# Performance work log

Measured on AMD Instinct MI355X. Metric: run time of the kernel, lower is better.

Reference implementation:

```python
import jax, jax.numpy as jnp
import numpy as np

STRIDE = 1
PADDING = 1

def setup_inputs() -> dict:
    key = jax.random.key(0)
    k1, k2 = jax.random.split(key)
    x = jax.random.normal(k1, (32, 128, 56, 56), dtype=jnp.float32)
    weight = jax.random.normal(k2, (256, 128, 3, 3), dtype=jnp.float32) * 0.01
    bias = jnp.zeros((256,), dtype=jnp.float32)
    return {"x": x, "weight": weight, "bias": bias}

def reference(x, weight, bias):
    # Same math as unfold (im2col) + matmul conv: a standard 2D cross-correlation.
    # Expressed as lax.conv_general_dilated, the efficient implicit-GEMM form.
    out = jax.lax.conv_general_dilated(
        x, weight,
        window_strides=(STRIDE, STRIDE),
        padding=[(PADDING, PADDING), (PADDING, PADDING)],
        dimension_numbers=("NCHW", "OIHW", "NCHW"),
    )
    out = out + bias[None, :, None, None]
    return out
```

## Files before the change

kernel.cpp:

```cpp
#include <hip/hip_runtime.h>

typedef int   v4i __attribute__((ext_vector_type(4)));
typedef float v4f __attribute__((ext_vector_type(4)));
typedef unsigned short ushort_t;

#define NB 32
#define CI 128
#define HW 56
#define KOC 256
#define HP 58
#define MTOT (NB*HW*HW)
#define XP_ELEMS ((size_t)NB*HP*HP*CI)
#define XP_OFF_BYTES ((size_t)1<<20)

__device__ __forceinline__ unsigned short f2bf(float f) {
    unsigned int u = __builtin_bit_cast(unsigned int, f);
    u += 0x7fffu + ((u >> 16) & 1u);
    return (unsigned short)(u >> 16);
}

__device__ __forceinline__ void gload16(const void* g, void* l) {
    __builtin_amdgcn_global_load_lds(
        (const __attribute__((address_space(1))) void*)g,
        (__attribute__((address_space(3))) void*)l, 16, 0, 0);
}

__global__ void wt_bf16(const float* __restrict__ w, ushort_t* __restrict__ wb) {
    int t = blockIdx.x * 256 + threadIdx.x;
    if (t >= KOC * CI) return;
    const float* src = w + (size_t)t * 9;
    int ko = t >> 7, c = t & 127;
    #pragma unroll
    for (int rs = 0; rs < 9; ++rs)
        wb[(size_t)(rs * KOC + ko) * CI + c] = f2bf(src[rs]);
}

__global__ void pad_nhwc_bf16(const float* __restrict__ x, ushort_t* __restrict__ xp) {
    __shared__ ushort_t tile[HW][136];
    int b = blockIdx.x;
    int n = b / HW, h = b % HW;
    int tid = threadIdx.x;
    const float* xr = x + (size_t)n * CI * HW * HW + (size_t)h * HW;
    for (int idx = tid; idx < CI * HW; idx += 256) {
        int c = idx / HW, w = idx % HW;
        tile[w][c] = f2bf(xr[(size_t)c * (HW * HW) + w]);
    }
    __syncthreads();
    ushort_t* xpr = xp + ((size_t)(n * HP + (h + 1)) * HP + 1) * CI;
    for (int idx = tid; idx < (HW * CI) / 8; idx += 256) {
        int w = idx >> 4, c8 = (idx & 15) * 8;
        *reinterpret_cast<uint4*>(xpr + (size_t)w * CI + c8) =
            *reinterpret_cast<const uint4*>(&tile[w][c8]);
    }
}

__global__ void border_zero(ushort_t* __restrict__ xp) {
    int t = blockIdx.x * 256 + threadIdx.x;
    if (t >= NB * 228 * 16) return;
    int c16 = t & 15;
    int p = (t >> 4) % 228;
    int n = t / (228 * 16);
    int h, wc;
    if (p < 58)       { h = 0;               wc = p; }
    else if (p < 116) { h = 57;              wc = p - 58; }
    else { int q = p - 116; h = 1 + (q >> 1); wc = (q & 1) * 57; }
    size_t off = ((size_t)(n * HP + h) * HP + wc) * CI + (size_t)c16 * 8;
    uint4 z; z.x = z.y = z.z = z.w = 0u;
    *reinterpret_cast<uint4*>(xp + off) = z;
}


#define BODY(POFF, IT, DO_STAGE) do {                                             \
    if (DO_STAGE) {                                                               \
        const int itn = (IT) + 1;                                                 \
        const int rsn = itn >> 2, cn = (itn & 3) * 32;                            \
        const int rn = (rsn * 11) >> 5, sn = rsn - rn * 3;                        \
        const size_t woffn = (size_t)rsn * (KOC * CI) + cn;                       \
        const size_t xoffn = (size_t)(rn * HP + sn) * CI + cn;                    \
        char* dst = ldsBase + ((POFF) ^ 16384);                                   \
        gload16(wb + wS0 + woffn, dst);                                           \
        gload16(wb + wS1 + woffn, dst + 4096);                                    \
        gload16(xp + xS0 + xoffn, dst + 8192);                                    \
        gload16(xp + xS1 + xoffn, dst + 12288);                                   \
    }                                                                             \
    _Pragma("unroll")                                                             \
    for (int a = 0; a < 4; ++a)                                                   \
        asm volatile("ds_read_b128 %0, %1 offset:" #POFF                          \
                     : "=v"(af[a]) : "v"(aAddr[a]));                              \
    _Pragma("unroll")                                                             \
    for (int b = 0; b < 4; ++b)                                                   \
        asm volatile("ds_read_b128 %0, %1 offset:" #POFF                          \
                     : "=v"(bf[b]) : "v"(bAddr[b]));                              \
    asm volatile("s_waitcnt lgkmcnt(0)");                                         \
    __builtin_amdgcn_sched_barrier(0);                                            \
    __builtin_amdgcn_s_setprio(1);                                                \
    _Pragma("unroll")                                                             \
    for (int a = 0; a < 4; ++a)                                                   \
        _Pragma("unroll")                                                         \
        for (int b = 0; b < 4; ++b)                                               \
            asm volatile("v_mfma_f32_16x16x32_bf16 %0, %1, %2, %0"                \
                         : "+v"(acc[a][b]) : "v"(af[a]), "v"(bf[b]));             \
    __builtin_amdgcn_s_setprio(0);                                                \
    asm volatile("s_waitcnt vmcnt(0)");                                           \
    __builtin_amdgcn_s_barrier();                                                 \
} while (0)

__global__ __launch_bounds__(256, 4) void conv_mfma(
    const ushort_t* __restrict__ xp,
    const ushort_t* __restrict__ wb,
    const float* __restrict__ bias,
    float* __restrict__ out)
{
    __shared__ alignas(16) ushort_t sAB[2][8192];

    const int tid  = threadIdx.x;
    const int lane = tid & 63;
    const int wv   = tid >> 6;
    const int wko  = wv >> 1, wm = wv & 1;
    const int bid   = blockIdx.x;
    const int chunk = (bid & 7) * 196 + (bid >> 3);
    const int mt = chunk >> 1, kt = chunk & 1;
    const int m0 = mt * 128, ko0 = kt * 128;
    const int lm = lane & 15, lk = lane >> 4;

    const int sc   = (lane & 3) ^ ((lane >> 3) & 3);
    const int row0 = wv * 16 + (lane >> 2);
    const size_t wS0 = (size_t)(ko0 + row0) * CI + sc * 8;
    const size_t wS1 = (size_t)(ko0 + 64 + row0) * CI + sc * 8;
    size_t xS0, xS1;
    {
        int mm = m0 + row0;
        int n = mm / 3136, tt = mm % 3136, oh = tt / 56, ow = tt % 56;
        xS0 = ((size_t)(n * HP + oh) * HP + ow) * CI + sc * 8;
        mm = m0 + 64 + row0;
        n = mm / 3136; tt = mm % 3136; oh = tt / 56; ow = tt % 56;
        xS1 = ((size_t)(n * HP + oh) * HP + ow) * CI + sc * 8;
    }
    char* ldsBase = (char*)&sAB[0][0] + wv * 1024;

    unsigned aAddr[4], bAddr[4];
    #pragma unroll
    for (int a = 0; a < 4; ++a) {
        int row = wko * 64 + a * 16 + lm;
        aAddr[a] = (unsigned)(size_t)&sAB[0][0]
                 + (unsigned)(row * 64 + (lk ^ ((row >> 1) & 3)) * 16);
    }
    #pragma unroll
    for (int b = 0; b < 4; ++b) {
        int row = wm * 64 + b * 16 + lm;
        bAddr[b] = (unsigned)(size_t)&sAB[0][0] + 8192u
                 + (unsigned)(row * 64 + (lk ^ ((row >> 1) & 3)) * 16);
    }

    v4f acc[4][4];
    const v4f vzero = {0.f, 0.f, 0.f, 0.f};
    #pragma unroll
    for (int a = 0; a < 4; ++a)
        #pragma unroll
        for (int b = 0; b < 4; ++b) acc[a][b] = vzero;

    v4i af[4], bf[4];

    gload16(wb + wS0, ldsBase);
    gload16(wb + wS1, ldsBase + 4096);
    gload16(xp + xS0, ldsBase + 8192);
    gload16(xp + xS1, ldsBase + 12288);
    asm volatile("s_waitcnt vmcnt(0)");
    __builtin_amdgcn_s_barrier();

    for (int t = 0; t < 17; ++t) {
        BODY(0,     2 * t,     true);
        BODY(16384, 2 * t + 1, true);
    }
    BODY(0,     34, true);
    BODY(16384, 35, false);

    asm volatile("s_nop 7\n\ts_nop 7\n\ts_nop 7"
        : "+v"(acc[0][0]), "+v"(acc[0][1]), "+v"(acc[0][2]), "+v"(acc[0][3]),
          "+v"(acc[1][0]), "+v"(acc[1][1]), "+v"(acc[1][2]), "+v"(acc[1][3]),
          "+v"(acc[2][0]), "+v"(acc[2][1]), "+v"(acc[2][2]), "+v"(acc[2][3]),
          "+v"(acc[3][0]), "+v"(acc[3][1]), "+v"(acc[3][2]), "+v"(acc[3][3]));

    const int koB = ko0 + wko * 64 + lk * 4;
    v4f bv[4];
    #pragma unroll
    for (int a = 0; a < 4; ++a)
        bv[a] = *reinterpret_cast<const v4f*>(bias + koB + a * 16);

    #pragma unroll
    for (int bb = 0; bb < 4; ++bb) {
        int mcol = m0 + wm * 64 + bb * 16 + lm;
        int n = mcol / 3136, t4 = mcol % 3136, oh = t4 / 56, ow = t4 % 56;
        size_t obase = (size_t)n * (KOC * 3136) + (size_t)oh * 56 + ow;
        #pragma unroll
        for (int a = 0; a < 4; ++a) {
            int kk = koB + a * 16;
            #pragma unroll
            for (int r = 0; r < 4; ++r)
                out[obase + (size_t)(kk + r) * 3136] = acc[a][bb][r] + bv[a][r];
        }
    }
}

__global__ void conv_naive(const float* __restrict__ x, const float* __restrict__ w,
                           const float* __restrict__ bias, float* __restrict__ out) {
    int idx = blockIdx.x * 256 + threadIdx.x;
    if (idx >= NB * KOC * HW * HW) return;
    int ow = idx % 56, t = idx / 56, oh = t % 56, t2 = t / 56, ko = t2 % 256, n = t2 / 256;
    float accv = bias[ko];
    for (int c = 0; c < CI; ++c)
        for (int r = 0; r < 3; ++r) {
            int ih = oh - 1 + r;
            if (ih < 0 || ih >= HW) continue;
            for (int s = 0; s < 3; ++s) {
                int iw = ow - 1 + s;
                if (iw < 0 || iw >= HW) continue;
                accv += x[((size_t)(n * CI + c) * HW + ih) * HW + iw] *
                        w[((size_t)(ko * CI + c) * 3 + r) * 3 + s];
            }
        }
    out[idx] = accv;
}

extern "C" void kernel_launch(void* const* d_in, const int* in_sizes, int n_in,
                              void* d_out, int out_size, void* d_ws, size_t ws_size,
                              hipStream_t stream) {
    const float* x    = (const float*)d_in[0];
    const float* w    = (const float*)d_in[1];
    const float* bias = (const float*)d_in[2];
    float* out = (float*)d_out;

    size_t need = XP_OFF_BYTES + XP_ELEMS * 2;
    if (ws_size < need) {
        int tot = NB * KOC * HW * HW;
        conv_naive<<<dim3((tot + 255) / 256), dim3(256), 0, stream>>>(x, w, bias, out);
        return;
    }

    ushort_t* wbp = (ushort_t*)d_ws;
    ushort_t* xpd = (ushort_t*)((char*)d_ws + XP_OFF_BYTES);

    border_zero<<<dim3((NB * 228 * 16 + 255) / 256), dim3(256), 0, stream>>>(xpd);
    wt_bf16<<<dim3((KOC * CI + 255) / 256), dim3(256), 0, stream>>>(w, wbp);
    pad_nhwc_bf16<<<dim3(NB * HW), dim3(256), 0, stream>>>(x, xpd);

    conv_mfma<<<dim3((MTOT / 128) * 2), dim3(256), 0, stream>>>(xpd, wbp, bias, out);
}
```

Baseline: 105.3 us.

## Split A/X LDS buffers and prefetch activations two stages ahead

Separates the weight and activation LDS tiles into a double-buffered A buffer and a triple-buffered X buffer. Activation loads are now issued two iterations ahead, and the per-iteration wait is relaxed from vmcnt(0) to vmcnt(2), so the gather-like activation loads overlap more MFMA work. The cost is more LDS (40KB vs 32KB), which could limit occupancy, plus more complex wait-count bookkeeping that must stay correct.

Result: no change. 104.5 us (-0.7%).

```diff
diff --git a/kernel.cpp b/kernel.cpp
--- a/kernel.cpp
+++ b/kernel.cpp
@@ -70,29 +70,39 @@
 }
 
 
-#define BODY(POFF, IT, DO_STAGE) do {                                             \
-    if (DO_STAGE) {                                                               \
+#define VMW(n) asm volatile("s_waitcnt vmcnt(" #n ")")
+#define SCHB() __builtin_amdgcn_sched_barrier(0)
+
+#define BODY(AOFF, XOFF, IT, DO_A, DO_X, VMSTMT, DO_BAR) do {                     \
+    if (DO_A) {                                                                   \
         const int itn = (IT) + 1;                                                 \
-        const int rsn = itn >> 2, cn = (itn & 3) * 32;                            \
-        const int rn = (rsn * 11) >> 5, sn = rsn - rn * 3;                        \
-        const size_t woffn = (size_t)rsn * (KOC * CI) + cn;                       \
-        const size_t xoffn = (size_t)(rn * HP + sn) * CI + cn;                    \
-        char* dst = ldsBase + ((POFF) ^ 16384);                                   \
-        gload16(wb + wS0 + woffn, dst);                                           \
-        gload16(wb + wS1 + woffn, dst + 4096);                                    \
-        gload16(xp + xS0 + xoffn, dst + 8192);                                    \
-        gload16(xp + xS1 + xoffn, dst + 12288);                                   \
+        const int rsn = itn >> 2;                                                 \
+        const size_t woffn = (size_t)rsn * (KOC * CI) + (itn & 3) * 32;           \
+        char* dA_ = baseA + ((itn) & 1) * 8192;                                   \
+        gload16(wb + wS0 + woffn, dA_);                                           \
+        gload16(wb + wS1 + woffn, dA_ + 4096);                                    \
     }                                                                             \
+    SCHB();                     \
+    if (DO_X) {                                                                   \
+        const int itx = (IT) + 2;                                                 \
+        const int rsx = itx >> 2;                                                 \
+        const int rx = (rsx * 11) >> 5, sx = rsx - rx * 3;                        \
+        const size_t xoffn = (size_t)(rx * HP + sx) * CI + (itx & 3) * 32;        \
+        char* dX_ = baseX + ((itx) % 3) * 8192;                                   \
+        gload16(xp + xS0 + xoffn, dX_);                                           \
+        gload16(xp + xS1 + xoffn, dX_ + 4096);                                    \
+    }                                                                             \
+    SCHB();                                                                       \
     _Pragma("unroll")                                                             \
     for (int a = 0; a < 4; ++a)                                                   \
-        asm volatile("ds_read_b128 %0, %1 offset:" #POFF                          \
+        asm volatile("ds_read_b128 %0, %1 offset:" #AOFF                          \
                      : "=v"(af[a]) : "v"(aAddr[a]));                              \
     _Pragma("unroll")                                                             \
     for (int b = 0; b < 4; ++b)                                                   \
-        asm volatile("ds_read_b128 %0, %1 offset:" #POFF                          \
-                     : "=v"(bf[b]) : "v"(bAddr[b]));                              \
+        asm volatile("ds_read_b128 %0, %1 offset:" #XOFF                          \
+                     : "=v"(bf[b]) : "v"(xAddr[b]));                              \
     asm volatile("s_waitcnt lgkmcnt(0)");                                         \
-    __builtin_amdgcn_sched_barrier(0);                                            \
+    SCHB();                                                                       \
     __builtin_amdgcn_s_setprio(1);                                                \
     _Pragma("unroll")                                                             \
     for (int a = 0; a < 4; ++a)                                                   \
@@ -101,8 +111,8 @@
             asm volatile("v_mfma_f32_16x16x32_bf16 %0, %1, %2, %0"                \
                          : "+v"(acc[a][b]) : "v"(af[a]), "v"(bf[b]));             \
     __builtin_amdgcn_s_setprio(0);                                                \
-    asm volatile("s_waitcnt vmcnt(0)");                                           \
-    __builtin_amdgcn_s_barrier();                                                 \
+    VMSTMT;                                                                       \
+    if (DO_BAR) __builtin_amdgcn_s_barrier();                                     \
 } while (0)
 
 __global__ __launch_bounds__(256, 4) void conv_mfma(
@@ -111,7 +121,8 @@
     const float* __restrict__ bias,
     float* __restrict__ out)
 {
-    __shared__ alignas(16) ushort_t sAB[2][8192];
+    __shared__ alignas(16) ushort_t sA[2][4096];
+    __shared__ alignas(16) ushort_t sX[3][4096];
 
     const int tid  = threadIdx.x;
     const int lane = tid & 63;
@@ -136,19 +147,20 @@
         n = mm / 3136; tt = mm % 3136; oh = tt / 56; ow = tt % 56;
         xS1 = ((size_t)(n * HP + oh) * HP + ow) * CI + sc * 8;
     }
-    char* ldsBase = (char*)&sAB[0][0] + wv * 1024;
-
-    unsigned aAddr[4], bAddr[4];
+    char* baseA = (char*)&sA[0][0] + wv * 1024;
+    char* baseX = (char*)&sX[0][0] + wv * 1024;
+
+    unsigned aAddr[4], xAddr[4];
     #pragma unroll
     for (int a = 0; a < 4; ++a) {
         int row = wko * 64 + a * 16 + lm;
-        aAddr[a] = (unsigned)(size_t)&sAB[0][0]
+        aAddr[a] = (unsigned)(size_t)&sA[0][0]
                  + (unsigned)(row * 64 + (lk ^ ((row >> 1) & 3)) * 16);
     }
     #pragma unroll
     for (int b = 0; b < 4; ++b) {
         int row = wm * 64 + b * 16 + lm;
-        bAddr[b] = (unsigned)(size_t)&sAB[0][0] + 8192u
+        xAddr[b] = (unsigned)(size_t)&sX[0][0]
                  + (unsigned)(row * 64 + (lk ^ ((row >> 1) & 3)) * 16);
     }
 
@@ -161,19 +173,32 @@
 
     v4i af[4], bf[4];
 
-    gload16(wb + wS0, ldsBase);
-    gload16(wb + wS1, ldsBase + 4096);
-    gload16(xp + xS0, ldsBase + 8192);
-    gload16(xp + xS1, ldsBase + 12288);
-    asm volatile("s_waitcnt vmcnt(0)");
+    gload16(wb + wS0, baseA);
+    gload16(wb + wS1, baseA + 4096);
+    SCHB();
+    gload16(xp + xS0, baseX);
+    gload16(xp + xS1, baseX + 4096);
+    gload16(xp + xS0 + 32, baseX + 8192);
+    gload16(xp + xS1 + 32, baseX + 8192 + 4096);
+    SCHB();
+    VMW(2);
     __builtin_amdgcn_s_barrier();
 
-    for (int t = 0; t < 17; ++t) {
-        BODY(0,     2 * t,     true);
-        BODY(16384, 2 * t + 1, true);
-    }
-    BODY(0,     34, true);
-    BODY(16384, 35, false);
+    for (int s = 0; s < 5; ++s) {
+        const int ib = 6 * s;
+        BODY(0,    0,     ib + 0, 1, 1, VMW(2), 1);
+        BODY(8192, 8192,  ib + 1, 1, 1, VMW(2), 1);
+        BODY(0,    16384, ib + 2, 1, 1, VMW(2), 1);
+        BODY(8192, 0,     ib + 3, 1, 1, VMW(2), 1);
+        BODY(0,    8192,  ib + 4, 1, 1, VMW(2), 1);
+        BODY(8192, 16384, ib + 5, 1, 1, VMW(2), 1);
+    }
+    BODY(0,    0,     30, 1, 1, VMW(2), 1);
+    BODY(8192, 8192,  31, 1, 1, VMW(2), 1);
+    BODY(0,    16384, 32, 1, 1, VMW(2), 1);
+    BODY(8192, 0,     33, 1, 1, VMW(2), 1);
+    BODY(0,    8192,  34, 1, 0, VMW(0), 1);
+    BODY(8192, 16384, 35, 0, 0, (void)0, 0);
 
     asm volatile("s_nop 7\n\ts_nop 7\n\ts_nop 7"
         : "+v"(acc[0][0]), "+v"(acc[0][1]), "+v"(acc[0][2]), "+v"(acc[0][3]),
```
